# Kernel tuning notes

Measured on AMD Instinct MI355X. Metric: run time of the kernel, lower is better.

Reference implementation:

```python
import jax, jax.numpy as jnp
import numpy as np
import math

B, M, L = 128, 16, 120          # bags, sentences per bag, tokens per sentence
V, WE, PE = 114042, 50, 5       # vocab, word embed, pos embed
PV = 2 * 30 + 1                 # pos vocab = pos_limit*2+1
OC, R, W = 230, 53, 3           # conv out channels, relations, window
D = WE + 2 * PE                 # input_size = 60


def setup_inputs() -> dict:
    key = jax.random.key(0)
    ks = jax.random.split(key, 10)
    con = math.sqrt(6.0 / (OC + R))
    con1 = math.sqrt(6.0 / ((PE + WE) * W))
    word_ids = jax.random.randint(ks[0], (B, M, L), 0, V)
    pos1_ids = jax.random.randint(ks[1], (B, M, L), 0, PV)
    pos2_ids = jax.random.randint(ks[2], (B, M, L), 0, PV)
    w2v = jax.random.normal(ks[3], (V, WE), dtype=jnp.float32) * 0.1
    pos_embed = jax.random.normal(ks[4], (PV, PE), dtype=jnp.float32) * 0.1
    conv_w = jax.random.uniform(ks[5], (OC, 1, W, D), dtype=jnp.float32, minval=-con1, maxval=con1)
    conv_bias = jax.random.uniform(ks[6], (1, OC), dtype=jnp.float32, minval=-con1, maxval=con1)
    r_embed = jax.random.uniform(ks[7], (R, OC), dtype=jnp.float32, minval=-con, maxval=con)
    r_bias = jax.random.uniform(ks[8], (R,), dtype=jnp.float32, minval=-con, maxval=con)
    att_W = jnp.broadcast_to(jnp.eye(OC, dtype=jnp.float32), (R, OC, OC)) + 0.0
    return {
        "word_ids": word_ids, "pos1_ids": pos1_ids, "pos2_ids": pos2_ids,
        "w2v": w2v, "pos_embed": pos_embed, "conv_w": conv_w,
        "conv_bias": conv_bias, "r_embed": r_embed, "r_bias": r_bias,
        "att_W": att_W,
    }


def reference(word_ids, pos1_ids, pos2_ids, w2v, pos_embed, conv_w,
              conv_bias, r_embed, r_bias, att_W):
    b, m, l = word_ids.shape
    oc = conv_w.shape[0]
    # embedding lookups + concat -> [B, M, L, D]
    x = jnp.concatenate([w2v[word_ids], pos_embed[pos1_ids], pos_embed[pos2_ids]], axis=-1)
    x = x.reshape(b * m, 1, l, x.shape[-1])
    # Conv2d(1, OC, (3, D), padding=(2, 0)) -> [B*M, OC, L+2, 1]
    y = jax.lax.conv_general_dilated(
        x, conv_w, window_strides=(1, 1), padding=[(W - 1, W - 1), (0, 0)],
        dimension_numbers=("NCHW", "OIHW", "NCHW"))
    # max-pool over time, add bias, tanh (dropout is identity in eval)
    feat = jnp.tanh(jnp.max(y[..., 0], axis=-1) + conv_bias[0])  # [B*M, OC]
    feat = feat.reshape(b, m, oc)
    # relation-specific bilinear attention: score[b,r,m] = r_e[r] @ att_W[r] @ feat[b,m]
    att_scores = jnp.einsum("rc,rcd,bmd->brm", r_embed, att_W, feat)
    att = jax.nn.softmax(att_scores, axis=-1)
    s = jnp.einsum("brm,bmc->brc", att, feat) * 0.5  # eval-mode explicit *0.5
    logits = jnp.einsum("brc,sc->brs", s, r_embed) + r_bias  # [B, R, R]
    pred = jnp.max(jax.nn.log_softmax(logits, axis=-1), axis=1)  # [B, R]
    return pred
```

## Files before the change

### kernel.cpp

```cpp
#include <hip/hip_runtime.h>
#include <hip/hip_bf16.h>
#include <math.h>

typedef __attribute__((ext_vector_type(8))) short bf16x8;
typedef __attribute__((ext_vector_type(4))) float f32x4;

#define NBAG 128
#define MM 16
#define LL 120
#define WEMB 50
#define PEMB 5
#define PV 61
#define OC 230
#define RR 53
#define DD 60

#define XPAD 72
#define XROWS 132
#define FSTRIDE 280
#define KP2 256

#define PREPB 12
#define QB 212
#define SPB 8

static __device__ __forceinline__ unsigned f2bfu(float v) {
    __hip_bfloat16 b = __float2bfloat16(v);
    return (unsigned)*reinterpret_cast<unsigned short*>(&b);
}
#define PK(lo, hi) (f2bfu(lo) | (f2bfu(hi) << 16))

static __device__ __forceinline__ void gload_lds16(const void* g, void* l) {
    __builtin_amdgcn_global_load_lds(
        (const __attribute__((address_space(1))) void*)g,
        (__attribute__((address_space(3))) void*)l, 16, 0, 0);
}

__global__ __launch_bounds__(512) void kernelA(
    const float* __restrict__ cw, const float* __restrict__ attW,
    const float* __restrict__ re, const float* __restrict__ pemb,
    __hip_bfloat16* __restrict__ wsB, float* __restrict__ qf,
    uint4* __restrict__ pemb16)
{
    __shared__ float part[2][256];
    int tid = threadIdx.x;
    int bid = blockIdx.x;

    if (bid < PREPB) {
        int t = bid * 512 + tid;
        if (t < 4 * 6 * 4 * 64) {
            int lane = t & 63, frag = t >> 6;
            int nt = frag & 3, rem = frag >> 2;
            int ks = rem % 6, oq = rem / 6;
            int oc = oq * 64 + nt * 16 + (lane & 15);
            int k0 = ks * 32 + (lane >> 4) * 8;
            bf16x8 o;
            #pragma unroll
            for (int e = 0; e < 8; ++e) {
                int k = k0 + e, kh = k >> 6, d = k & 63;
                float v = (oc < OC && d < DD) ? cw[oc * (3 * DD) + kh * DD + d] : 0.f;
                o[e] = (short)f2bfu(v);
            }
            ((bf16x8*)wsB)[t] = o;
        }
        if (bid == 0 && tid < PV) {
            const float* e = pemb + tid * PEMB;
            uint4 o;
            o.x = PK(e[0], e[1]);
            o.y = PK(e[2], e[3]);
            o.z = f2bfu(e[4]);
            o.w = 0u;
            pemb16[tid] = o;
        }
        return;
    }

    int qb = bid - PREPB;
    int r = qb >> 2, qt = qb & 3;
    int cs = tid >> 8, d = tid & 255;
    int c0 = qt * 58 + cs * 29;
    int c1 = min(OC, qt * 58 + (cs + 1) * 29);
    const float* W = attW + (size_t)r * OC * OC;
    const float* rer = re + r * OC;
    float acc = 0.f;
    if (d < OC)
        for (int c = c0; c < c1; ++c) acc += rer[c] * W[(size_t)c * OC + d];
    part[cs][d] = acc;
    __syncthreads();
    if (cs == 0 && d < OC)
        qf[qt * (RR * OC) + r * OC + d] = part[0][d] + part[1][d];
}

__global__ __launch_bounds__(512, 2) void convW(
    const int* __restrict__ wid, const int* __restrict__ p1, const int* __restrict__ p2,
    const float* __restrict__ w2v, const uint4* __restrict__ pemb16,
    const __hip_bfloat16* __restrict__ wsB, const float* __restrict__ cb,
    const float* __restrict__ qf, const float* __restrict__ re,
    __hip_bfloat16* __restrict__ wsB2, __hip_bfloat16* __restrict__ feat16)
{
    __shared__ __align__(16) __hip_bfloat16 wlds[4 * 6 * 4 * 64 * 8];
    __shared__ __align__(16) __hip_bfloat16 xs[2][XROWS * XPAD];
    __shared__ float sm[2][2][256];
    int tid = threadIdx.x, lane = tid & 63, wave = tid >> 6;
    int s0 = blockIdx.x * SPB;

    {
        const char* gw = (const char*)wsB;
        char* lw = (char*)wlds;
        #pragma unroll
        for (int i = 0; i < 12; ++i) {
            int off = i * 8192 + wave * 1024 + lane * 16;
            gload_lds16(gw + off, lw + i * 8192 + wave * 1024);
        }
    }

    int row = tid >> 1, h = tid & 1;
    bool stager = tid < XROWS * 2;
    bool valid = stager && row >= 2 && row < 122;
    int j = row - 2;
    int idw[SPB + 2], id1[SPB + 2], id2[SPB + 2];
    if (valid) {
        #pragma unroll
        for (int s = 0; s < SPB; ++s) {
            int base = (s0 + s) * LL + j;
            idw[s] = wid[base];
            if (h) { id1[s] = p1[base]; id2[s] = p2[base]; }
        }
    }
    float2 ga, gb, gc, gd, ge, gf_, gg, gh_, gi, gj, gk, gl, gm;
    uint4 e1r, e2r;

#define LD(s)                                                                   \
    if (valid) {                                                                \
        const float* wr = w2v + (size_t)idw[s] * WEMB + (h ? 24 : 0);           \
        ga = *(const float2*)(wr + 0);   gb = *(const float2*)(wr + 2);         \
        gc = *(const float2*)(wr + 4);   gd = *(const float2*)(wr + 6);         \
        ge = *(const float2*)(wr + 8);   gf_ = *(const float2*)(wr + 10);       \
        gg = *(const float2*)(wr + 12);  gh_ = *(const float2*)(wr + 14);       \
        gi = *(const float2*)(wr + 16);  gj = *(const float2*)(wr + 18);        \
        gk = *(const float2*)(wr + 20);  gl = *(const float2*)(wr + 22);        \
        if (h) { gm = *(const float2*)(wr + 24);                                \
                 e1r = pemb16[id1[s]];  e2r = pemb16[id2[s]]; }                 \
    }

#define ST(buf)                                                                 \
    if (stager) {                                                               \
        uint4* dst = (uint4*)&xs[buf][row * XPAD];                              \
        const uint4 z = make_uint4(0u, 0u, 0u, 0u);                             \
        if (valid) {                                                            \
            if (h == 0) {                                                       \
                uint4 o0, o1, o2;                                               \
                o0.x = PK(ga.x, ga.y);  o0.y = PK(gb.x, gb.y);                  \
                o0.z = PK(gc.x, gc.y);  o0.w = PK(gd.x, gd.y);                  \
                o1.x = PK(ge.x, ge.y);  o1.y = PK(gf_.x, gf_.y);                \
                o1.z = PK(gg.x, gg.y);  o1.w = PK(gh_.x, gh_.y);                \
                o2.x = PK(gi.x, gi.y);  o2.y = PK(gj.x, gj.y);                  \
                o2.z = PK(gk.x, gk.y);  o2.w = PK(gl.x, gl.y);                  \
                dst[0] = o0; dst[1] = o1; dst[2] = o2;                          \
            } else {                                                            \
                uint4 o3, o4, o5, o6, o7;                                       \
                o3.x = PK(ga.x, ga.y);  o3.y = PK(gb.x, gb.y);                  \
                o3.z = PK(gc.x, gc.y);  o3.w = PK(gd.x, gd.y);                  \
                o4.x = PK(ge.x, ge.y);  o4.y = PK(gf_.x, gf_.y);                \
                o4.z = PK(gg.x, gg.y);  o4.w = PK(gh_.x, gh_.y);                \
                o5.x = PK(gi.x, gi.y);  o5.y = PK(gj.x, gj.y);                  \
                o5.z = PK(gk.x, gk.y);  o5.w = PK(gl.x, gl.y);                  \
                o6.x = PK(gm.x, gm.y);  o6.y = e1r.x;  o6.z = e1r.y;            \
                o6.w = (e1r.z & 0xFFFFu) | (e2r.x << 16);                       \
                o7.x = (e2r.x >> 16) | (e2r.y << 16);                           \
                o7.y = (e2r.y >> 16) | (e2r.z << 16);                           \
                o7.z = 0u; o7.w = 0u;                                           \
                dst[3] = o3; dst[4] = o4; dst[5] = o5;                          \
                dst[6] = o6; dst[7] = o7; dst[8] = z;                           \
            }                                                                   \
        } else {                                                                \
            if (h == 0) { dst[0]=z; dst[1]=z; dst[2]=z; dst[3]=z; dst[4]=z; }   \
            else        { dst[5]=z; dst[6]=z; dst[7]=z; dst[8]=z; }             \
        }                                                                       \
    }

    LD(0)
    ST(0)
    LD(1)

    {
        int ptid = tid - XROWS * 2;
        if (ptid >= 0 && ptid < 16) {
            int t = blockIdx.x * 16 + ptid;
            int plane = t & 63, f = t >> 6;
            int ks = f >> 3, nt = f & 7;
            int col = nt * 16 + (plane & 15);
            int k0 = ks * 32 + (plane >> 4) * 8;
            bf16x8 o;
            #pragma unroll
            for (int e = 0; e < 8; ++e) {
                int k = k0 + e;
                float v = 0.f;
                if (k < OC) {
                    if (col < RR)
                        v = qf[col * OC + k] + qf[RR * OC + col * OC + k]
                          + qf[2 * RR * OC + col * OC + k] + qf[3 * RR * OC + col * OC + k];
                    else if (col >= 64 && col < 64 + RR)
                        v = re[(col - 64) * OC + k];
                }
                o[e] = (short)f2bfu(v);
            }
            ((bf16x8*)wsB2)[t] = o;
        }
    }
    __syncthreads();

    int oq = wave >> 1, th = wave & 1;
    int lr = lane & 15, lh = lane >> 4;
    const bf16x8* wb = (const bf16x8*)wlds;

    #pragma unroll
    for (int i = 0; i < SPB; ++i) {
        const int cur = i & 1;
        if (i + 1 < SPB) {
            ST(cur ^ 1)
            if (i + 2 < SPB) { LD(i + 2) }
        }

        f32x4 acc[4][4];
        #pragma unroll
        for (int a = 0; a < 4; ++a)
            #pragma unroll
            for (int b = 0; b < 4; ++b) acc[a][b] = (f32x4){0.f, 0.f, 0.f, 0.f};

        const __hip_bfloat16* xsc = xs[cur];
        #pragma unroll
        for (int ks = 0; ks < 6; ++ks) {
            bf16x8 bfrag[4];
            #pragma unroll
            for (int nt = 0; nt < 4; ++nt)
                bfrag[nt] = wb[((oq * 6 + ks) * 4 + nt) * 64 + lane];
            int k = ks * 32 + lh * 8;
            int kh = k >> 6, d = k & 63;
            #pragma unroll
            for (int mt = 0; mt < 4; ++mt) {
                int xrow = th * 64 + mt * 16 + lr + kh;
                bf16x8 af = *(const bf16x8*)&xsc[xrow * XPAD + d];
                #pragma unroll
                for (int nt = 0; nt < 4; ++nt)
                    acc[mt][nt] = __builtin_amdgcn_mfma_f32_16x16x32_bf16(af, bfrag[nt], acc[mt][nt], 0, 0, 0);
            }
        }

        #pragma unroll
        for (int nt = 0; nt < 4; ++nt) {
            float mx = -1e30f;
            #pragma unroll
            for (int mt = 0; mt < 4; ++mt) {
                #pragma unroll
                for (int r = 0; r < 4; ++r) {
                    int t = th * 64 + mt * 16 + lh * 4 + r;
                    if (t < 122) mx = fmaxf(mx, acc[mt][nt][r]);
                }
            }
            mx = fmaxf(mx, __shfl_xor(mx, 16));
            mx = fmaxf(mx, __shfl_xor(mx, 32));
            if (lane < 16) sm[cur][th][oq * 64 + nt * 16 + lr] = mx;
        }
        __syncthreads();
        if (tid < KP2) {
            float v = (tid < OC) ? tanhf(fmaxf(sm[cur][0][tid], sm[cur][1][tid]) + cb[tid]) : 0.f;
            feat16[(size_t)(s0 + i) * FSTRIDE + tid] = __float2bfloat16(v);
        }
    }
#undef LD
#undef ST
}

__global__ __launch_bounds__(512) void bag_kernel(
    const __hip_bfloat16* __restrict__ feat16, const __hip_bfloat16* __restrict__ wsB2,
    const float* __restrict__ rb, float* __restrict__ out)
{
    __shared__ __hip_bfloat16 fA[MM * FSTRIDE];
    __shared__ float scg[MM][132];
    __shared__ float att[RR][17];
    __shared__ float lg[RR * 56];
    __shared__ float lse[RR];
    int b = blockIdx.x, tid = threadIdx.x;
    int lane = tid & 63, wave = tid >> 6;
    int lr = lane & 15, lh = lane >> 4;

    const char* gf = (const char*)(feat16 + (size_t)b * MM * FSTRIDE);
    char* lf = (char*)fA;
    #pragma unroll
    for (int i = 0; i < 2; ++i) {
        int off = i * 8192 + wave * 1024 + lane * 16;
        if (off < MM * FSTRIDE * 2) gload_lds16(gf + off, lf + i * 8192 + wave * 1024);
    }
    __syncthreads();

    f32x4 acc = (f32x4){0.f, 0.f, 0.f, 0.f};
    const bf16x8* wb2 = (const bf16x8*)wsB2;
    #pragma unroll
    for (int ks = 0; ks < 8; ++ks) {
        bf16x8 bfrag = wb2[(ks * 8 + wave) * 64 + lane];
        int k = ks * 32 + lh * 8;
        bf16x8 af = *(const bf16x8*)((const char*)fA + lr * (FSTRIDE * 2) + k * 2);
        acc = __builtin_amdgcn_mfma_f32_16x16x32_bf16(af, bfrag, acc, 0, 0, 0);
    }
    #pragma unroll
    for (int r = 0; r < 4; ++r) scg[lh * 4 + r][wave * 16 + lr] = acc[r];
    __syncthreads();

    if (tid < RR) {
        float mx = -1e30f;
        #pragma unroll
        for (int m = 0; m < MM; ++m) mx = fmaxf(mx, scg[m][tid]);
        float s = 0.f, e[MM];
        #pragma unroll
        for (int m = 0; m < MM; ++m) { e[m] = expf(scg[m][tid] - mx); s += e[m]; }
        float inv = 1.f / s;
        #pragma unroll
        for (int m = 0; m < MM; ++m) att[tid][m] = e[m] * inv;
    }
    __syncthreads();

    for (int idx = tid; idx < RR * RR; idx += 512) {
        int r = idx % RR, s2 = idx / RR;
        float a = 0.f;
        #pragma unroll
        for (int m = 0; m < MM; ++m) a += att[r][m] * scg[m][64 + s2];
        lg[r * 56 + s2] = 0.5f * a + rb[s2];
    }
    __syncthreads();

    if (tid < RR) {
        float mx = -1e30f;
        for (int s2 = 0; s2 < RR; ++s2) mx = fmaxf(mx, lg[tid * 56 + s2]);
        float s = 0.f;
        for (int s2 = 0; s2 < RR; ++s2) s += expf(lg[tid * 56 + s2] - mx);
        lse[tid] = mx + logf(s);
    }
    __syncthreads();

    if (tid < RR) {
        float mx = -1e30f;
        for (int r = 0; r < RR; ++r) mx = fmaxf(mx, lg[r * 56 + tid] - lse[r]);
        out[b * RR + tid] = mx;
    }
}

extern "C" void kernel_launch(void* const* d_in, const int* in_sizes, int n_in,
                              void* d_out, int out_size, void* d_ws, size_t ws_size,
                              hipStream_t stream) {
    const int* wid   = (const int*)d_in[0];
    const int* p1    = (const int*)d_in[1];
    const int* p2    = (const int*)d_in[2];
    const float* w2v = (const float*)d_in[3];
    const float* pe  = (const float*)d_in[4];
    const float* cw  = (const float*)d_in[5];
    const float* cb  = (const float*)d_in[6];
    const float* re  = (const float*)d_in[7];
    const float* rb  = (const float*)d_in[8];
    const float* attW= (const float*)d_in[9];
    float* out = (float*)d_out;

    float* qf            = (float*)d_ws;
    __hip_bfloat16* wsB  = (__hip_bfloat16*)((char*)d_ws + 196608);
    __hip_bfloat16* wsB2 = (__hip_bfloat16*)((char*)d_ws + 294912);
    __hip_bfloat16* f16  = (__hip_bfloat16*)((char*)d_ws + 360448);
    uint4* pemb16        = (uint4*)((char*)d_ws + 1507328);

    kernelA<<<PREPB + QB, 512, 0, stream>>>(cw, attW, re, pe, wsB, qf, pemb16);
    convW<<<256, 512, 0, stream>>>(wid, p1, p2, w2v, pemb16, wsB, cb,
                                   qf, re, wsB2, f16);
    bag_kernel<<<NBAG, 512, 0, stream>>>(f16, wsB2, rb, out);
}
```

Measured before the change: 52.43 us.

## Fold attention query projection into conv kernel, shrink prep kernel

Computes the relation query vectors (r_embed times att_W) inside the conv kernel instead of in a separate 212-block prep kernel. Otherwise-idle staging threads in each conv block handle a slice, writing bf16 values straight into the MFMA fragment layout and zeroing the padding. This drops the fp32 qf intermediate and its reduction step, and the first kernel becomes a small 12-block weight-reformat launch. The cost is that the dot-product work (a 230-step strided loop per element) now sits on the conv kernel's prologue path before its first barrier.

```diff
diff --git a/kernel.cpp b/kernel.cpp
--- a/kernel.cpp
+++ b/kernel.cpp
@@ -21,7 +21,6 @@
 #define KP2 256
 
 #define PREPB 12
-#define QB 212
 #define SPB 8
 
 static __device__ __forceinline__ unsigned f2bfu(float v) {
@@ -36,73 +35,52 @@
         (__attribute__((address_space(3))) void*)l, 16, 0, 0);
 }
 
-__global__ __launch_bounds__(512) void kernelA(
-    const float* __restrict__ cw, const float* __restrict__ attW,
-    const float* __restrict__ re, const float* __restrict__ pemb,
-    __hip_bfloat16* __restrict__ wsB, float* __restrict__ qf,
-    uint4* __restrict__ pemb16)
+__global__ __launch_bounds__(512) void prepK(
+    const float* __restrict__ cw, const float* __restrict__ pemb,
+    __hip_bfloat16* __restrict__ wsB, uint4* __restrict__ pemb16)
 {
-    __shared__ float part[2][256];
     int tid = threadIdx.x;
     int bid = blockIdx.x;
-
-    if (bid < PREPB) {
-        int t = bid * 512 + tid;
-        if (t < 4 * 6 * 4 * 64) {
-            int lane = t & 63, frag = t >> 6;
-            int nt = frag & 3, rem = frag >> 2;
-            int ks = rem % 6, oq = rem / 6;
-            int oc = oq * 64 + nt * 16 + (lane & 15);
-            int k0 = ks * 32 + (lane >> 4) * 8;
-            bf16x8 o;
-            #pragma unroll
-            for (int e = 0; e < 8; ++e) {
-                int k = k0 + e, kh = k >> 6, d = k & 63;
-                float v = (oc < OC && d < DD) ? cw[oc * (3 * DD) + kh * DD + d] : 0.f;
-                o[e] = (short)f2bfu(v);
-            }
-            ((bf16x8*)wsB)[t] = o;
-        }
-        if (bid == 0 && tid < PV) {
-            const float* e = pemb + tid * PEMB;
-            uint4 o;
-            o.x = PK(e[0], e[1]);
-            o.y = PK(e[2], e[3]);
-            o.z = f2bfu(e[4]);
-            o.w = 0u;
-            pemb16[tid] = o;
-        }
-        return;
-    }
-
-    int qb = bid - PREPB;
-    int r = qb >> 2, qt = qb & 3;
-    int cs = tid >> 8, d = tid & 255;
-    int c0 = qt * 58 + cs * 29;
-    int c1 = min(OC, qt * 58 + (cs + 1) * 29);
-    const float* W = attW + (size_t)r * OC * OC;
-    const float* rer = re + r * OC;
-    float acc = 0.f;
-    if (d < OC)
-        for (int c = c0; c < c1; ++c) acc += rer[c] * W[(size_t)c * OC + d];
-    part[cs][d] = acc;
-    __syncthreads();
-    if (cs == 0 && d < OC)
-        qf[qt * (RR * OC) + r * OC + d] = part[0][d] + part[1][d];
+    int t = bid * 512 + tid;
+    if (t < 4 * 6 * 4 * 64) {
+        int lane = t & 63, frag = t >> 6;
+        int nt = frag & 3, rem = frag >> 2;
+        int ks = rem % 6, oq = rem / 6;
+        int oc = oq * 64 + nt * 16 + (lane & 15);
+        int k0 = ks * 32 + (lane >> 4) * 8;
+        bf16x8 o;
+        #pragma unroll
+        for (int e = 0; e < 8; ++e) {
+            int k = k0 + e, kh = k >> 6, d = k & 63;
+            float v = (oc < OC && d < DD) ? cw[oc * (3 * DD) + kh * DD + d] : 0.f;
+            o[e] = (short)f2bfu(v);
+        }
+        ((bf16x8*)wsB)[t] = o;
+    }
+    if (bid == 0 && tid < PV) {
+        const float* e = pemb + tid * PEMB;
+        uint4 o;
+        o.x = PK(e[0], e[1]);
+        o.y = PK(e[2], e[3]);
+        o.z = f2bfu(e[4]);
+        o.w = 0u;
+        pemb16[tid] = o;
+    }
 }
 
 __global__ __launch_bounds__(512, 2) void convW(
     const int* __restrict__ wid, const int* __restrict__ p1, const int* __restrict__ p2,
     const float* __restrict__ w2v, const uint4* __restrict__ pemb16,
     const __hip_bfloat16* __restrict__ wsB, const float* __restrict__ cb,
-    const float* __restrict__ qf, const float* __restrict__ re,
+    const float* __restrict__ attW, const float* __restrict__ re,
     __hip_bfloat16* __restrict__ wsB2, __hip_bfloat16* __restrict__ feat16)
 {
     __shared__ __align__(16) __hip_bfloat16 wlds[4 * 6 * 4 * 64 * 8];
     __shared__ __align__(16) __hip_bfloat16 xs[2][XROWS * XPAD];
     __shared__ float sm[2][2][256];
     int tid = threadIdx.x, lane = tid & 63, wave = tid >> 6;
-    int s0 = blockIdx.x * SPB;
+    int bid = blockIdx.x;
+    int s0 = bid * SPB;
 
     {
         const char* gw = (const char*)wsB;
@@ -180,34 +158,60 @@
     }
 
     LD(0)
+
+    if (tid >= 280 && tid < 328) {
+        int g = bid * 48 + (tid - 280);
+        if (g < RR * OC) {
+            int r = g / OC, d = g - r * OC;
+            const float* W = attW + (size_t)r * OC * OC + d;
+            const float* rr_ = re + r * OC;
+            float a0 = 0.f, a1 = 0.f, a2 = 0.f, a3 = 0.f;
+            int c = 0;
+            for (; c + 4 <= OC; c += 4) {
+                a0 += rr_[c]     * W[(size_t)c * OC];
+                a1 += rr_[c + 1] * W[(size_t)(c + 1) * OC];
+                a2 += rr_[c + 2] * W[(size_t)(c + 2) * OC];
+                a3 += rr_[c + 3] * W[(size_t)(c + 3) * OC];
+            }
+            for (; c < OC; ++c) a0 += rr_[c] * W[(size_t)c * OC];
+            float qv = (a0 + a1) + (a2 + a3);
+            int ks = d >> 5, e = d & 7, nt = r >> 4;
+            int ln = (r & 15) | (((d >> 3) & 3) << 4);
+            wsB2[((((ks * 8 + nt) * 64 + ln)) << 3) + e] = __float2bfloat16(qv);
+        }
+    }
+    if (tid >= 328 && tid < 376) {
+        int g = bid * 48 + (tid - 328);
+        if (g < RR * OC) {
+            int r = g / OC, d = g - r * OC;
+            int col = 64 + r;
+            int ks = d >> 5, e = d & 7, nt = col >> 4;
+            int ln = (col & 15) | (((d >> 3) & 3) << 4);
+            wsB2[((((ks * 8 + nt) * 64 + ln)) << 3) + e] = __float2bfloat16(re[r * OC + d]);
+        }
+    }
+    if (bid < 22 && tid >= 376 && tid < 408) {
+        int col = (bid < 11) ? (53 + bid) : (106 + bid);
+        int s = tid - 376;
+        int ks = s >> 2, l4 = s & 3;
+        int ln = (col & 15) | (l4 << 4), nt = col >> 4;
+        ((uint4*)wsB2)[(ks * 8 + nt) * 64 + ln] = make_uint4(0u, 0u, 0u, 0u);
+    }
+    if (bid >= 22 && bid < 128 && tid >= 376 && tid < 408) {
+        int gcol = bid - 22;
+        int col = (gcol < RR) ? gcol : (64 + gcol - RR);
+        int s = tid - 376;
+        if (s < 26) {
+            int l4, e;
+            if (s < 2) { l4 = 0; e = 6 + s; }
+            else       { int u = s - 2; l4 = 1 + (u >> 3); e = u & 7; }
+            int ln = (col & 15) | (l4 << 4), nt = col >> 4;
+            wsB2[((((7 * 8 + nt) * 64 + ln)) << 3) + e] = __float2bfloat16(0.f);
+        }
+    }
+
     ST(0)
     LD(1)
-
-    {
-        int ptid = tid - XROWS * 2;
-        if (ptid >= 0 && ptid < 16) {
-            int t = blockIdx.x * 16 + ptid;
-            int plane = t & 63, f = t >> 6;
-            int ks = f >> 3, nt = f & 7;
-            int col = nt * 16 + (plane & 15);
-            int k0 = ks * 32 + (plane >> 4) * 8;
-            bf16x8 o;
-            #pragma unroll
-            for (int e = 0; e < 8; ++e) {
-                int k = k0 + e;
-                float v = 0.f;
-                if (k < OC) {
-                    if (col < RR)
-                        v = qf[col * OC + k] + qf[RR * OC + col * OC + k]
-                          + qf[2 * RR * OC + col * OC + k] + qf[3 * RR * OC + col * OC + k];
-                    else if (col >= 64 && col < 64 + RR)
-                        v = re[(col - 64) * OC + k];
-                }
-                o[e] = (short)f2bfu(v);
-            }
-            ((bf16x8*)wsB2)[t] = o;
-        }
-    }
     __syncthreads();
 
     int oq = wave >> 1, th = wave & 1;
@@ -360,14 +364,13 @@
     const float* attW= (const float*)d_in[9];
     float* out = (float*)d_out;
 
-    float* qf            = (float*)d_ws;
-    __hip_bfloat16* wsB  = (__hip_bfloat16*)((char*)d_ws + 196608);
-    __hip_bfloat16* wsB2 = (__hip_bfloat16*)((char*)d_ws + 294912);
-    __hip_bfloat16* f16  = (__hip_bfloat16*)((char*)d_ws + 360448);
-    uint4* pemb16        = (uint4*)((char*)d_ws + 1507328);
-
-    kernelA<<<PREPB + QB, 512, 0, stream>>>(cw, attW, re, pe, wsB, qf, pemb16);
+    __hip_bfloat16* wsB  = (__hip_bfloat16*)d_ws;
+    __hip_bfloat16* wsB2 = (__hip_bfloat16*)((char*)d_ws + 98304);
+    __hip_bfloat16* f16  = (__hip_bfloat16*)((char*)d_ws + 163840);
+    uint4* pemb16        = (uint4*)((char*)d_ws + 1310720);
+
+    prepK<<<PREPB, 512, 0, stream>>>(cw, pe, wsB, pemb16);
     convW<<<256, 512, 0, stream>>>(wid, p1, p2, w2v, pemb16, wsB, cb,
-                                   qf, re, wsB2, f16);
+                                   attW, re, wsB2, f16);
     bag_kernel<<<NBAG, 512, 0, stream>>>(f16, wsB2, rb, out);
 }
```

Result: slower. 61.83 us (+17.9%).

## Hold conv weight fragments in registers instead of LDS, load ids lazily

Applied to the files above, without the earlier changes.

Each wave now loads its conv weight B-fragments (6x4 bf16x8) straight from global memory into registers once, instead of staging the whole weight tile in LDS and re-reading it for every sentence. This removes about 96KB of LDS per block and the per-iteration LDS weight reads. The token id arrays are no longer preloaded into registers; ids are read inside each embedding load. The min-blocks launch bound is dropped, which lets the compiler spend more registers per thread but may lower occupancy. It also adds a dependent id-then-row global load chain per sentence.

```diff
diff --git a/kernel.cpp b/kernel.cpp
--- a/kernel.cpp
+++ b/kernel.cpp
@@ -91,48 +91,42 @@
         qf[qt * (RR * OC) + r * OC + d] = part[0][d] + part[1][d];
 }
 
-__global__ __launch_bounds__(512, 2) void convW(
+__global__ __launch_bounds__(512) void convW(
     const int* __restrict__ wid, const int* __restrict__ p1, const int* __restrict__ p2,
     const float* __restrict__ w2v, const uint4* __restrict__ pemb16,
     const __hip_bfloat16* __restrict__ wsB, const float* __restrict__ cb,
     const float* __restrict__ qf, const float* __restrict__ re,
     __hip_bfloat16* __restrict__ wsB2, __hip_bfloat16* __restrict__ feat16)
 {
-    __shared__ __align__(16) __hip_bfloat16 wlds[4 * 6 * 4 * 64 * 8];
     __shared__ __align__(16) __hip_bfloat16 xs[2][XROWS * XPAD];
     __shared__ float sm[2][2][256];
     int tid = threadIdx.x, lane = tid & 63, wave = tid >> 6;
-    int s0 = blockIdx.x * SPB;
-
+    int bid = blockIdx.x;
+    int s0 = bid * SPB;
+    int oq = wave >> 1, th = wave & 1;
+
+    bf16x8 wreg[6][4];
     {
-        const char* gw = (const char*)wsB;
-        char* lw = (char*)wlds;
-        #pragma unroll
-        for (int i = 0; i < 12; ++i) {
-            int off = i * 8192 + wave * 1024 + lane * 16;
-            gload_lds16(gw + off, lw + i * 8192 + wave * 1024);
-        }
+        const bf16x8* wb = (const bf16x8*)wsB;
+        #pragma unroll
+        for (int ks = 0; ks < 6; ++ks)
+            #pragma unroll
+            for (int nt = 0; nt < 4; ++nt)
+                wreg[ks][nt] = wb[((oq * 6 + ks) * 4 + nt) * 64 + lane];
     }
 
     int row = tid >> 1, h = tid & 1;
     bool stager = tid < XROWS * 2;
     bool valid = stager && row >= 2 && row < 122;
     int j = row - 2;
-    int idw[SPB + 2], id1[SPB + 2], id2[SPB + 2];
-    if (valid) {
-        #pragma unroll
-        for (int s = 0; s < SPB; ++s) {
-            int base = (s0 + s) * LL + j;
-            idw[s] = wid[base];
-            if (h) { id1[s] = p1[base]; id2[s] = p2[base]; }
-        }
-    }
     float2 ga, gb, gc, gd, ge, gf_, gg, gh_, gi, gj, gk, gl, gm;
     uint4 e1r, e2r;
 
 #define LD(s)                                                                   \
     if (valid) {                                                                \
-        const float* wr = w2v + (size_t)idw[s] * WEMB + (h ? 24 : 0);           \
+        int base = (s0 + (s)) * LL + j;                                         \
+        int iw = wid[base];                                                     \
+        const float* wr = w2v + (size_t)iw * WEMB + (h ? 24 : 0);               \
         ga = *(const float2*)(wr + 0);   gb = *(const float2*)(wr + 2);         \
         gc = *(const float2*)(wr + 4);   gd = *(const float2*)(wr + 6);         \
         ge = *(const float2*)(wr + 8);   gf_ = *(const float2*)(wr + 10);       \
@@ -140,7 +134,7 @@
         gi = *(const float2*)(wr + 16);  gj = *(const float2*)(wr + 18);        \
         gk = *(const float2*)(wr + 20);  gl = *(const float2*)(wr + 22);        \
         if (h) { gm = *(const float2*)(wr + 24);                                \
-                 e1r = pemb16[id1[s]];  e2r = pemb16[id2[s]]; }                 \
+                 e1r = pemb16[p1[base]];  e2r = pemb16[p2[base]]; }             \
     }
 
 #define ST(buf)                                                                 \
@@ -186,7 +180,7 @@
     {
         int ptid = tid - XROWS * 2;
         if (ptid >= 0 && ptid < 16) {
-            int t = blockIdx.x * 16 + ptid;
+            int t = bid * 16 + ptid;
             int plane = t & 63, f = t >> 6;
             int ks = f >> 3, nt = f & 7;
             int col = nt * 16 + (plane & 15);
@@ -210,9 +204,7 @@
     }
     __syncthreads();
 
-    int oq = wave >> 1, th = wave & 1;
     int lr = lane & 15, lh = lane >> 4;
-    const bf16x8* wb = (const bf16x8*)wlds;
 
     #pragma unroll
     for (int i = 0; i < SPB; ++i) {
@@ -231,10 +223,6 @@
         const __hip_bfloat16* xsc = xs[cur];
         #pragma unroll
         for (int ks = 0; ks < 6; ++ks) {
-            bf16x8 bfrag[4];
-            #pragma unroll
-            for (int nt = 0; nt < 4; ++nt)
-                bfrag[nt] = wb[((oq * 6 + ks) * 4 + nt) * 64 + lane];
             int k = ks * 32 + lh * 8;
             int kh = k >> 6, d = k & 63;
             #pragma unroll
@@ -243,7 +231,7 @@
                 bf16x8 af = *(const bf16x8*)&xsc[xrow * XPAD + d];
                 #pragma unroll
                 for (int nt = 0; nt < 4; ++nt)
-                    acc[mt][nt] = __builtin_amdgcn_mfma_f32_16x16x32_bf16(af, bfrag[nt], acc[mt][nt], 0, 0, 0);
+                    acc[mt][nt] = __builtin_amdgcn_mfma_f32_16x16x32_bf16(af, wreg[ks][nt], acc[mt][nt], 0, 0, 0);
             }
         }
 
```

Result: slower. 56.36 us (+7.5%).
